# Kernel optimization log

Hardware: AMD Instinct MI355X
Metric: run time of the kernel (lower is better)

## Reference

```python
import jax, jax.numpy as jnp
import numpy as np
import math

N_TOTAL = 262144
C = 128
B = 512
LMAX = 512  # max segment length (static for jit)


def setup_inputs() -> dict:
    key = jax.random.key(0)
    ks = jax.random.split(key, 8)
    Q_feature = jax.random.normal(ks[0], (N_TOTAL, C), dtype=jnp.float32)
    K_feature = jax.random.normal(ks[1], (N_TOTAL, C), dtype=jnp.float32)
    # cumulative offsets: equal segments of length LMAX (general code handles ragged)
    offset = (jnp.arange(1, B + 1, dtype=jnp.int64) * (N_TOTAL // B))
    s = 1.0 / math.sqrt(C)
    Wq = jax.random.normal(ks[2], (C, C), dtype=jnp.float32) * s
    Wk = jax.random.normal(ks[3], (C, C), dtype=jnp.float32) * s
    Wv = jax.random.normal(ks[4], (C, C), dtype=jnp.float32) * s
    bq = jnp.zeros((C,), dtype=jnp.float32)
    bk = jnp.zeros((C,), dtype=jnp.float32)
    bv = jnp.zeros((C,), dtype=jnp.float32)
    return {"Q_feature": Q_feature, "K_feature": K_feature,
            "Wq": Wq, "bq": bq, "Wk": Wk, "bk": bk, "Wv": Wv, "bv": bv,
            "offset": offset}


def reference(Q_feature, K_feature, Wq, bq, Wk, bk, Wv, bv, offset):
    N, Cdim = Q_feature.shape
    Q = Q_feature @ Wq.T + bq
    K = K_feature @ Wk.T + bk
    V = K_feature @ Wv.T + bv

    starts = jnp.concatenate([jnp.zeros((1,), offset.dtype), offset[:-1]])
    lengths = offset - starts                         # (B,)
    pos = jnp.arange(LMAX)                            # (LMAX,)
    idx = jnp.clip(starts[:, None] + pos[None, :], 0, N - 1)  # (B, LMAX)
    mask = pos[None, :] < lengths[:, None]            # (B, LMAX) valid tokens

    Qp = Q[idx]                                       # (B, LMAX, C)
    Kp = K[idx]
    Vp = V[idx]

    scale = 1.0 / math.sqrt(Cdim)
    scores = jnp.einsum('blc,bmc->blm', Qp, Kp) * scale     # (B, LMAX, LMAX)
    scores = jnp.where(mask[:, None, :], scores, jnp.float32(-1e30))
    attn = jax.nn.softmax(scores, axis=-1)
    outp = jnp.einsum('blm,bmc->blc', attn, Vp)             # (B, LMAX, C)
    outp = outp * mask[:, :, None]                          # zero padded rows

    # scatter padded segments back to flat (N, C); idx is an exact partition on valid rows
    out = jnp.zeros((N, Cdim), dtype=outp.dtype).at[idx].add(outp)
    return out
```

## Files before the change

### kernel.cpp

```cpp
#include <hip/hip_runtime.h>
#include <hip/hip_bf16.h>

#define CDIM 128
#define LMAXC 512
#define QBLK 128
#define KVBLK 64

#define QSCALE (0.08838834764831845f * 1.4426950408889634f)

typedef __attribute__((ext_vector_type(8))) short bf16x8;
typedef __attribute__((ext_vector_type(4))) short bf16x4;
typedef __attribute__((ext_vector_type(4))) float f32x4;

__device__ inline short f2bf(float f) {
    union { float f; unsigned u; } v; v.f = f;
    unsigned r = v.u + 0x7FFFu + ((v.u >> 16) & 1u);
    return (short)(r >> 16);
}

__device__ inline bf16x8 cvt8v(float4 a, float4 b) {
    bf16x8 o;
    o[0] = f2bf(a.x); o[1] = f2bf(a.y); o[2] = f2bf(a.z); o[3] = f2bf(a.w);
    o[4] = f2bf(b.x); o[5] = f2bf(b.y); o[6] = f2bf(b.z); o[7] = f2bf(b.w);
    return o;
}

__device__ inline unsigned pk2(float lo, float hi) {
    unsigned r;
    asm("v_cvt_pk_bf16_f32 %0, %1, %2" : "=v"(r) : "v"(lo), "v"(hi));
    return r;
}

__device__ inline void gload16(const void* g, void* l) {
    __builtin_amdgcn_global_load_lds(
        (const __attribute__((address_space(1))) unsigned*)g,
        (__attribute__((address_space(3))) unsigned*)l, 16, 0, 0);
}

__device__ inline void blk_barrier() {
    __builtin_amdgcn_sched_barrier(0);
    __builtin_amdgcn_s_barrier();
    __builtin_amdgcn_sched_barrier(0);
}

__device__ inline int pch(int q) { return ((q + (q >> 3)) & 7) << 4; }

__global__ void wcvt_kernel(const float* __restrict__ Wq,
                            const float* __restrict__ Wk,
                            const float* __restrict__ Wv,
                            short* __restrict__ Wbf)
{
    int t = blockIdx.x * 256 + threadIdx.x;
    int m = t / 2048;
    int e = (t % 2048) * 8;
    const float* W = (m == 0) ? Wq : (m == 1) ? Wk : Wv;
    float sc = (m == 0) ? QSCALE : 1.0f;
    float4 a = *reinterpret_cast<const float4*>(W + e);
    float4 b = *reinterpret_cast<const float4*>(W + e + 4);
    a.x *= sc; a.y *= sc; a.z *= sc; a.w *= sc;
    b.x *= sc; b.y *= sc; b.z *= sc; b.w *= sc;
    *reinterpret_cast<bf16x8*>(Wbf + m * 16384 + e) = cvt8v(a, b);
}

__global__ __launch_bounds__(256) void proj_kernel(
    const float* __restrict__ Qf, const float* __restrict__ Kf,
    const short* __restrict__ Wbf,
    const float* __restrict__ bq, const float* __restrict__ bk,
    const float* __restrict__ bv,
    short* __restrict__ Qp, short* __restrict__ Kp, short* __restrict__ Vt,
    int N)
{
    __shared__ __align__(16) char wlds[32768];

    const int tid   = threadIdx.x;
    const int lane  = tid & 63;
    const int wv    = tid >> 6;
    const int lrow  = lane & 15;
    const int lhalf = lane >> 4;
    const int row0  = blockIdx.x * 128;
    const int which = blockIdx.y;
    const float* X  = (which == 0) ? Qf : Kf;
    const short* Wg = Wbf + which * 16384;

#pragma unroll
    for (int j = 0; j < 8; ++j) {
        int beta = j * 4096 + tid * 16;
        int r  = beta >> 8;
        int gs = ((beta >> 4) & 15) ^ (r & 7);
        gload16(Wg + r * 128 + gs * 8, wlds + beta);
    }

    bf16x8 xfr[2][4];
#pragma unroll
    for (int xt = 0; xt < 2; ++xt) {
        const float* xr = X + (size_t)(row0 + wv * 32 + xt * 16 + lrow) * CDIM;
#pragma unroll
        for (int ks = 0; ks < 4; ++ks) {
            const float4* s = reinterpret_cast<const float4*>(xr + ks * 32 + lhalf * 8);
            xfr[xt][ks] = cvt8v(s[0], s[1]);
        }
    }
    __syncthreads();

    if (which < 2) {
        const float* bias = (which == 0) ? bq : bk;
        const float  bsc  = (which == 0) ? QSCALE : 1.0f;
        short* outp       = (which == 0) ? Qp : Kp;

#pragma unroll
        for (int cf = 0; cf < 8; ++cf) {
            const int key = cf * 16 + lrow;
            bf16x8 wfr[4];
#pragma unroll
            for (int ks = 0; ks < 4; ++ks) {
                int wb = (key * 256 + (ks * 32 + lhalf * 8) * 2) ^ ((key & 7) << 4);
                wfr[ks] = *reinterpret_cast<const bf16x8*>(wlds + wb);
            }
            float4 bv4 = *reinterpret_cast<const float4*>(bias + cf * 16 + lhalf * 4);
#pragma unroll
            for (int xt = 0; xt < 2; ++xt) {
                f32x4 acc = {0.f, 0.f, 0.f, 0.f};
#pragma unroll
                for (int ks = 0; ks < 4; ++ks)
                    acc = __builtin_amdgcn_mfma_f32_16x16x32_bf16(wfr[ks], xfr[xt][ks], acc, 0, 0, 0);
                bf16x4 pk;
                pk[0] = f2bf(acc[0] + bv4.x * bsc);
                pk[1] = f2bf(acc[1] + bv4.y * bsc);
                pk[2] = f2bf(acc[2] + bv4.z * bsc);
                pk[3] = f2bf(acc[3] + bv4.w * bsc);
                *reinterpret_cast<bf16x4*>(
                    outp + (size_t)(row0 + wv * 32 + xt * 16 + lrow) * CDIM
                         + cf * 16 + lhalf * 4) = pk;
            }
        }
    } else {
#pragma unroll
        for (int cf = 0; cf < 8; ++cf) {
            const int d = cf * 16 + lrow;
            bf16x8 wfr[4];
#pragma unroll
            for (int ks = 0; ks < 4; ++ks) {
                int wb = (d * 256 + (ks * 32 + lhalf * 8) * 2) ^ ((d & 7) << 4);
                wfr[ks] = *reinterpret_cast<const bf16x8*>(wlds + wb);
            }
            f32x4 acc0 = {0.f, 0.f, 0.f, 0.f};
            f32x4 acc1 = {0.f, 0.f, 0.f, 0.f};
#pragma unroll
            for (int ks = 0; ks < 4; ++ks) {
                acc0 = __builtin_amdgcn_mfma_f32_16x16x32_bf16(xfr[0][ks], wfr[ks], acc0, 0, 0, 0);
                acc1 = __builtin_amdgcn_mfma_f32_16x16x32_bf16(xfr[1][ks], wfr[ks], acc1, 0, 0, 0);
            }
            float bcol = bv[d];
            bf16x4 p0, p1;
#pragma unroll
            for (int r = 0; r < 4; ++r) {
                p0[r] = f2bf(acc0[r] + bcol);
                p1[r] = f2bf(acc1[r] + bcol);
            }
            short* vrow = Vt + (size_t)d * N + row0 + wv * 32 + lhalf * 4;
            *reinterpret_cast<bf16x4*>(vrow)      = p0;
            *reinterpret_cast<bf16x4*>(vrow + 16) = p1;
        }
    }
}

__global__ __launch_bounds__(256) void attn_kernel(
    const short* __restrict__ Qp, const short* __restrict__ Kp,
    const short* __restrict__ VtG, const int* __restrict__ offset,
    float* __restrict__ out, int Ntot)
{
    __shared__ __align__(16) char smem[81920];
    char* lds_p = smem + 65536;

    const int nq = LMAXC / QBLK;
    int flat = blockIdx.x, total = gridDim.x;
    int seg, qb;
    if ((total & (8 * nq - 1)) == 0) {
        int per = total >> 3;
        int xcd = flat & 7;
        int wi  = flat >> 3;
        int sl  = wi / nq;
        qb  = wi - sl * nq;
        seg = xcd * (per / nq) + sl;
    } else { seg = flat / nq; qb = flat - seg * nq; }

    const int start = (seg == 0) ? 0 : offset[seg - 1];
    int len = offset[seg] - start;
    if (len > LMAXC) len = LMAXC;
    const int q0 = qb * QBLK;
    if (q0 >= len) return;

    const int tid   = threadIdx.x;
    const int lane  = tid & 63;
    const int wv    = tid >> 6;
    const int lrow  = lane & 15;
    const int lhalf = lane >> 4;
    const int ntiles = (len + KVBLK - 1) / KVBLK;
    const int lm1 = len - 1;

    auto stage = [&](int kv0, int bb) {
        char* kb = smem + bb * 32768;
        char* vb = kb + 16384;
#pragma unroll
        for (int j = 0; j < 4; ++j) {
            int beta = j * 4096 + wv * 1024 + (lane << 4);
            int r  = beta >> 8;
            int gs = ((beta >> 4) & 15) ^ (r & 7);
            int rg = kv0 + r; if (rg > lm1) rg = lm1;
            gload16(Kp + (((size_t)(start + rg)) << 7) + (gs << 3),
                    kb + j * 4096 + wv * 1024);
            int d   = beta >> 7;
            int gs2 = ((beta >> 4) & 7) ^ (d & 7);
            long gk = (long)start + kv0 + (gs2 << 3);
            if (gk + 8 > Ntot) gk = Ntot - 8;
            gload16(VtG + (size_t)d * Ntot + gk,
                    vb + j * 4096 + wv * 1024);
        }
    };

    stage(0, 0);

    bf16x8 aq[2][4];
#pragma unroll
    for (int qt = 0; qt < 2; ++qt) {
        int qr = q0 + wv * 32 + qt * 16 + lrow;
        if (qr > lm1) qr = lm1;
        const short* qrow = Qp + (size_t)(start + qr) * CDIM;
#pragma unroll
        for (int ks = 0; ks < 4; ++ks)
            aq[qt][ks] = *reinterpret_cast<const bf16x8*>(qrow + ks * 32 + lhalf * 8);
    }

    f32x4 acc_o[2][8];
    float lsum[2] = {0.f, 0.f};
#pragma unroll
    for (int qt = 0; qt < 2; ++qt)
#pragma unroll
        for (int df = 0; df < 8; ++df) acc_o[qt][df] = (f32x4){0.f, 0.f, 0.f, 0.f};

    const int wbase = wv * 4096;

    for (int t = 0; t < ntiles; ++t) {
        const int kv0 = t * KVBLK;
        const int bb  = t & 1;
        if (t + 1 < ntiles) {
            stage(kv0 + KVBLK, bb ^ 1);
            asm volatile("s_waitcnt vmcnt(8)" ::: "memory");
        } else {
            asm volatile("s_waitcnt vmcnt(0)" ::: "memory");
        }
        blk_barrier();

        char* lds_k  = smem + bb * 32768;
        char* lds_vt = lds_k + 16384;
        const bool tail = (kv0 + KVBLK > len);

        f32x4 s0[4], s1[4];
        __builtin_amdgcn_s_setprio(1);
#pragma unroll
        for (int kf = 0; kf < 4; ++kf) {
            s0[kf] = (f32x4){0.f, 0.f, 0.f, 0.f};
            s1[kf] = (f32x4){0.f, 0.f, 0.f, 0.f};
            int key = kf * 16 + lrow;
#pragma unroll
            for (int ks = 0; ks < 4; ++ks) {
                int kbo = (key * 256 + (ks * 32 + lhalf * 8) * 2) ^ ((key & 7) << 4);
                bf16x8 kfr = *reinterpret_cast<const bf16x8*>(lds_k + kbo);
                s0[kf] = __builtin_amdgcn_mfma_f32_16x16x32_bf16(kfr, aq[0][ks], s0[kf], 0, 0, 0);
                s1[kf] = __builtin_amdgcn_mfma_f32_16x16x32_bf16(kfr, aq[1][ks], s1[kf], 0, 0, 0);
            }
        }
        __builtin_amdgcn_s_setprio(0);

        const int keyb0 = kv0 + lhalf * 4;
#pragma unroll
        for (int qt = 0; qt < 2; ++qt) {
            const int qlocal = qt * 16 + lrow;
            const int rowoff = wbase + qlocal * 128;
            const int swz = pch(qlocal);
#pragma unroll
            for (int kf = 0; kf < 4; ++kf) {
                f32x4 sv = qt ? s1[kf] : s0[kf];
                float p[4];
#pragma unroll
                for (int r = 0; r < 4; ++r) {
                    float pv = exp2f(sv[r]);
                    if (tail && (keyb0 + kf * 16 + r >= len)) pv = 0.f;
                    p[r] = pv;
                    lsum[qt] += pv;
                }
                unsigned long long w =
                    (unsigned long long)pk2(p[0], p[1]) |
                    ((unsigned long long)pk2(p[2], p[3]) << 32);
                *reinterpret_cast<unsigned long long*>(
                    lds_p + rowoff + ((kf * 32 + lhalf * 8) ^ swz)) = w;
            }
        }

        __builtin_amdgcn_s_setprio(1);
#pragma unroll
        for (int ks2 = 0; ks2 < 2; ++ks2) {
            bf16x8 ap0 = *reinterpret_cast<const bf16x8*>(
                lds_p + wbase + lrow * 128 + ((ks2 * 64 + lhalf * 16) ^ pch(lrow)));
            bf16x8 ap1 = *reinterpret_cast<const bf16x8*>(
                lds_p + wbase + (16 + lrow) * 128 + ((ks2 * 64 + lhalf * 16) ^ pch(16 + lrow)));
            int k0 = ks2 * 32 + lhalf * 8;
#pragma unroll
            for (int df = 0; df < 8; ++df) {
                int d = df * 16 + lrow;
                int vb2 = (d * 128 + k0 * 2) ^ ((d & 7) << 4);
                bf16x8 bvf = *reinterpret_cast<const bf16x8*>(lds_vt + vb2);
                acc_o[0][df] = __builtin_amdgcn_mfma_f32_16x16x32_bf16(ap0, bvf, acc_o[0][df], 0, 0, 0);
                acc_o[1][df] = __builtin_amdgcn_mfma_f32_16x16x32_bf16(ap1, bvf, acc_o[1][df], 0, 0, 0);
            }
        }
        __builtin_amdgcn_s_setprio(0);

        blk_barrier();
    }

#pragma unroll
    for (int qt = 0; qt < 2; ++qt) {
        float l = lsum[qt];
        l += __shfl_xor(l, 16);
        l += __shfl_xor(l, 32);
        float rinv[4];
#pragma unroll
        for (int r = 0; r < 4; ++r)
            rinv[r] = 1.0f / __shfl(l, lhalf * 4 + r);
#pragma unroll
        for (int df = 0; df < 8; ++df)
#pragma unroll
            for (int r = 0; r < 4; ++r) {
                int qg = q0 + wv * 32 + qt * 16 + lhalf * 4 + r;
                if (qg < len)
                    out[(size_t)(start + qg) * CDIM + df * 16 + lrow]
                        = acc_o[qt][df][r] * rinv[r];
            }
    }
}

extern "C" void kernel_launch(void* const* d_in, const int* in_sizes, int n_in,
                              void* d_out, int out_size, void* d_ws, size_t ws_size,
                              hipStream_t stream) {
    const float* Qf = (const float*)d_in[0];
    const float* Kf = (const float*)d_in[1];
    const float* Wq = (const float*)d_in[2];
    const float* bq = (const float*)d_in[3];
    const float* Wk = (const float*)d_in[4];
    const float* bk = (const float*)d_in[5];
    const float* Wv = (const float*)d_in[6];
    const float* bv_ = (const float*)d_in[7];
    const int* offset = (const int*)d_in[8];

    const int N = in_sizes[0] / CDIM;
    const int B = in_sizes[8];

    short* Qp = (short*)d_ws;
    short* Kp = Qp + (size_t)N * CDIM;
    short* Vt = Kp + (size_t)N * CDIM;
    float* out = (float*)d_out;

    size_t base_need = (size_t)3 * N * CDIM * 2;
    short* Wbf = (ws_size >= base_need + 3 * 16384 * 2)
               ? (Vt + (size_t)N * CDIM) : (short*)d_out;

    wcvt_kernel<<<24, 256, 0, stream>>>(Wq, Wk, Wv, Wbf);

    dim3 pgrid(N / 128, 3);
    proj_kernel<<<pgrid, 256, 0, stream>>>(Qf, Kf, Wbf, bq, bk, bv_,
                                           Qp, Kp, Vt, N);

    attn_kernel<<<dim3(B * (LMAXC / QBLK)), 256, 0, stream>>>(
        Qp, Kp, Vt, offset, out, N);
}
```

Before: 254.0 us.

## Process four row tiles per projection block with software-prefetched inputs

Each projection block now handles 512 rows instead of 128. The weight tile staged in LDS is reused across four 128-row tiles, and the grid shrinks by four. The next tile's fp32 input is loaded into registers while MFMAs run on the current tile, so global load latency overlaps compute. The cost is higher register pressure from the raw float4 buffer, which may lower occupancy, and fewer blocks are available to fill the GPU.

```diff
diff --git a/kernel.cpp b/kernel.cpp
--- a/kernel.cpp
+++ b/kernel.cpp
@@ -62,6 +62,98 @@
     *reinterpret_cast<bf16x8*>(Wbf + m * 16384 + e) = cvt8v(a, b);
 }
 
+__device__ inline void loadraw(const float* __restrict__ X, int rowbase,
+                               int lrow, int lhalf, float4* raw)
+{
+#pragma unroll
+    for (int xt = 0; xt < 2; ++xt) {
+        const float* xr = X + (size_t)(rowbase + xt * 16 + lrow) * CDIM + lhalf * 8;
+#pragma unroll
+        for (int ks = 0; ks < 4; ++ks) {
+            raw[xt * 8 + ks * 2 + 0] = *reinterpret_cast<const float4*>(xr + ks * 32);
+            raw[xt * 8 + ks * 2 + 1] = *reinterpret_cast<const float4*>(xr + ks * 32 + 4);
+        }
+    }
+}
+
+__device__ inline void cvtraw(const float4* raw, bf16x8 xfr[2][4])
+{
+#pragma unroll
+    for (int xt = 0; xt < 2; ++xt)
+#pragma unroll
+        for (int ks = 0; ks < 4; ++ks)
+            xfr[xt][ks] = cvt8v(raw[xt * 8 + ks * 2], raw[xt * 8 + ks * 2 + 1]);
+}
+
+__device__ inline void tile_qk(const char* __restrict__ wlds,
+                               const bf16x8 xfr[2][4],
+                               const float* __restrict__ bias, float bsc,
+                               short* __restrict__ outp, int row0t,
+                               int lrow, int lhalf, int wv)
+{
+#pragma unroll
+    for (int cf = 0; cf < 8; ++cf) {
+        const int key = cf * 16 + lrow;
+        bf16x8 wfr[4];
+#pragma unroll
+        for (int ks = 0; ks < 4; ++ks) {
+            int wb = (key * 256 + (ks * 32 + lhalf * 8) * 2) ^ ((key & 7) << 4);
+            wfr[ks] = *reinterpret_cast<const bf16x8*>(wlds + wb);
+        }
+        float4 bv4 = *reinterpret_cast<const float4*>(bias + cf * 16 + lhalf * 4);
+#pragma unroll
+        for (int xt = 0; xt < 2; ++xt) {
+            f32x4 acc = {0.f, 0.f, 0.f, 0.f};
+#pragma unroll
+            for (int ks = 0; ks < 4; ++ks)
+                acc = __builtin_amdgcn_mfma_f32_16x16x32_bf16(wfr[ks], xfr[xt][ks], acc, 0, 0, 0);
+            bf16x4 pk;
+            pk[0] = f2bf(acc[0] + bv4.x * bsc);
+            pk[1] = f2bf(acc[1] + bv4.y * bsc);
+            pk[2] = f2bf(acc[2] + bv4.z * bsc);
+            pk[3] = f2bf(acc[3] + bv4.w * bsc);
+            *reinterpret_cast<bf16x4*>(
+                outp + (size_t)(row0t + wv * 32 + xt * 16 + lrow) * CDIM
+                     + cf * 16 + lhalf * 4) = pk;
+        }
+    }
+}
+
+__device__ inline void tile_v(const char* __restrict__ wlds,
+                              const bf16x8 xfr[2][4],
+                              const float* __restrict__ bv,
+                              short* __restrict__ Vt, int row0t, int N,
+                              int lrow, int lhalf, int wv)
+{
+#pragma unroll
+    for (int cf = 0; cf < 8; ++cf) {
+        const int d = cf * 16 + lrow;
+        bf16x8 wfr[4];
+#pragma unroll
+        for (int ks = 0; ks < 4; ++ks) {
+            int wb = (d * 256 + (ks * 32 + lhalf * 8) * 2) ^ ((d & 7) << 4);
+            wfr[ks] = *reinterpret_cast<const bf16x8*>(wlds + wb);
+        }
+        f32x4 acc0 = {0.f, 0.f, 0.f, 0.f};
+        f32x4 acc1 = {0.f, 0.f, 0.f, 0.f};
+#pragma unroll
+        for (int ks = 0; ks < 4; ++ks) {
+            acc0 = __builtin_amdgcn_mfma_f32_16x16x32_bf16(xfr[0][ks], wfr[ks], acc0, 0, 0, 0);
+            acc1 = __builtin_amdgcn_mfma_f32_16x16x32_bf16(xfr[1][ks], wfr[ks], acc1, 0, 0, 0);
+        }
+        float bcol = bv[d];
+        bf16x4 p0, p1;
+#pragma unroll
+        for (int r = 0; r < 4; ++r) {
+            p0[r] = f2bf(acc0[r] + bcol);
+            p1[r] = f2bf(acc1[r] + bcol);
+        }
+        short* vrow = Vt + (size_t)d * N + row0t + wv * 32 + lhalf * 4;
+        *reinterpret_cast<bf16x4*>(vrow)      = p0;
+        *reinterpret_cast<bf16x4*>(vrow + 16) = p1;
+    }
+}
+
 __global__ __launch_bounds__(256) void proj_kernel(
     const float* __restrict__ Qf, const float* __restrict__ Kf,
     const short* __restrict__ Wbf,
@@ -77,7 +169,7 @@
     const int wv    = tid >> 6;
     const int lrow  = lane & 15;
     const int lhalf = lane >> 4;
-    const int row0  = blockIdx.x * 128;
+    const int row0  = blockIdx.x * 512;
     const int which = blockIdx.y;
     const float* X  = (which == 0) ? Qf : Kf;
     const short* Wg = Wbf + which * 16384;
@@ -90,76 +182,32 @@
         gload16(Wg + r * 128 + gs * 8, wlds + beta);
     }
 
+    float4 raw[16];
     bf16x8 xfr[2][4];
-#pragma unroll
-    for (int xt = 0; xt < 2; ++xt) {
-        const float* xr = X + (size_t)(row0 + wv * 32 + xt * 16 + lrow) * CDIM;
-#pragma unroll
-        for (int ks = 0; ks < 4; ++ks) {
-            const float4* s = reinterpret_cast<const float4*>(xr + ks * 32 + lhalf * 8);
-            xfr[xt][ks] = cvt8v(s[0], s[1]);
-        }
-    }
+    loadraw(X, row0 + wv * 32, lrow, lhalf, raw);
+    cvtraw(raw, xfr);
     __syncthreads();
 
-    if (which < 2) {
-        const float* bias = (which == 0) ? bq : bk;
-        const float  bsc  = (which == 0) ? QSCALE : 1.0f;
-        short* outp       = (which == 0) ? Qp : Kp;
-
-#pragma unroll
-        for (int cf = 0; cf < 8; ++cf) {
-            const int key = cf * 16 + lrow;
-            bf16x8 wfr[4];
-#pragma unroll
-            for (int ks = 0; ks < 4; ++ks) {
-                int wb = (key * 256 + (ks * 32 + lhalf * 8) * 2) ^ ((key & 7) << 4);
-                wfr[ks] = *reinterpret_cast<const bf16x8*>(wlds + wb);
-            }
-            float4 bv4 = *reinterpret_cast<const float4*>(bias + cf * 16 + lhalf * 4);
-#pragma unroll
-            for (int xt = 0; xt < 2; ++xt) {
-                f32x4 acc = {0.f, 0.f, 0.f, 0.f};
-#pragma unroll
-                for (int ks = 0; ks < 4; ++ks)
-                    acc = __builtin_amdgcn_mfma_f32_16x16x32_bf16(wfr[ks], xfr[xt][ks], acc, 0, 0, 0);
-                bf16x4 pk;
-                pk[0] = f2bf(acc[0] + bv4.x * bsc);
-                pk[1] = f2bf(acc[1] + bv4.y * bsc);
-                pk[2] = f2bf(acc[2] + bv4.z * bsc);
-                pk[3] = f2bf(acc[3] + bv4.w * bsc);
-                *reinterpret_cast<bf16x4*>(
-                    outp + (size_t)(row0 + wv * 32 + xt * 16 + lrow) * CDIM
-                         + cf * 16 + lhalf * 4) = pk;
-            }
+    if (which == 0) {
+#pragma unroll
+        for (int t = 0; t < 4; ++t) {
+            if (t < 3) loadraw(X, row0 + (t + 1) * 128 + wv * 32, lrow, lhalf, raw);
+            tile_qk(wlds, xfr, bq, QSCALE, Qp, row0 + t * 128, lrow, lhalf, wv);
+            if (t < 3) cvtraw(raw, xfr);
+        }
+    } else if (which == 1) {
+#pragma unroll
+        for (int t = 0; t < 4; ++t) {
+            if (t < 3) loadraw(X, row0 + (t + 1) * 128 + wv * 32, lrow, lhalf, raw);
+            tile_qk(wlds, xfr, bk, 1.0f, Kp, row0 + t * 128, lrow, lhalf, wv);
+            if (t < 3) cvtraw(raw, xfr);
         }
     } else {
 #pragma unroll
-        for (int cf = 0; cf < 8; ++cf) {
-            const int d = cf * 16 + lrow;
-            bf16x8 wfr[4];
-#pragma unroll
-            for (int ks = 0; ks < 4; ++ks) {
-                int wb = (d * 256 + (ks * 32 + lhalf * 8) * 2) ^ ((d & 7) << 4);
-                wfr[ks] = *reinterpret_cast<const bf16x8*>(wlds + wb);
-            }
-            f32x4 acc0 = {0.f, 0.f, 0.f, 0.f};
-            f32x4 acc1 = {0.f, 0.f, 0.f, 0.f};
-#pragma unroll
-            for (int ks = 0; ks < 4; ++ks) {
-                acc0 = __builtin_amdgcn_mfma_f32_16x16x32_bf16(xfr[0][ks], wfr[ks], acc0, 0, 0, 0);
-                acc1 = __builtin_amdgcn_mfma_f32_16x16x32_bf16(xfr[1][ks], wfr[ks], acc1, 0, 0, 0);
-            }
-            float bcol = bv[d];
-            bf16x4 p0, p1;
-#pragma unroll
-            for (int r = 0; r < 4; ++r) {
-                p0[r] = f2bf(acc0[r] + bcol);
-                p1[r] = f2bf(acc1[r] + bcol);
-            }
-            short* vrow = Vt + (size_t)d * N + row0 + wv * 32 + lhalf * 4;
-            *reinterpret_cast<bf16x4*>(vrow)      = p0;
-            *reinterpret_cast<bf16x4*>(vrow + 16) = p1;
+        for (int t = 0; t < 4; ++t) {
+            if (t < 3) loadraw(X, row0 + (t + 1) * 128 + wv * 32, lrow, lhalf, raw);
+            tile_v(wlds, xfr, bv, Vt, row0 + t * 128, N, lrow, lhalf, wv);
+            if (t < 3) cvtraw(raw, xfr);
         }
     }
 }
@@ -367,7 +415,7 @@
 
     wcvt_kernel<<<24, 256, 0, stream>>>(Wq, Wk, Wv, Wbf);
 
-    dim3 pgrid(N / 128, 3);
+    dim3 pgrid(N / 512, 3);
     proj_kernel<<<pgrid, 256, 0, stream>>>(Qf, Kf, Wbf, bq, bk, bv_,
                                            Qp, Kp, Vt, N);
 
```

Result: slower. 282.4 us (+11.2%).

## Fuse K and V projections to reuse K_feature loads, use 512-thread blocks

Applied to the files above, without the earlier changes.

The projection kernel previously ran three grid slices (Q, K, V), each loading and converting its input rows from fp32. K and V both read K_feature, so that data was fetched twice. The K-slice blocks now compute K, reload the Wv tile into LDS after a barrier, and compute V from the same register-resident fragments, which removes the redundant read. Blocks also grow to 512 threads covering 256 rows. The cost is an extra LDS reload and two barriers in the K/V blocks, plus an uneven workload between Q blocks and K/V blocks.

```diff
diff --git a/kernel.cpp b/kernel.cpp
--- a/kernel.cpp
+++ b/kernel.cpp
@@ -62,7 +62,76 @@
     *reinterpret_cast<bf16x8*>(Wbf + m * 16384 + e) = cvt8v(a, b);
 }
 
-__global__ __launch_bounds__(256) void proj_kernel(
+__device__ inline void tile_qk(const char* __restrict__ wlds,
+                               const bf16x8 xfr[2][4],
+                               const float* __restrict__ bias, float bsc,
+                               short* __restrict__ outp, int rowb,
+                               int lrow, int lhalf)
+{
+#pragma unroll
+    for (int cf = 0; cf < 8; ++cf) {
+        const int key = cf * 16 + lrow;
+        bf16x8 wfr[4];
+#pragma unroll
+        for (int ks = 0; ks < 4; ++ks) {
+            int wb = (key * 256 + (ks * 32 + lhalf * 8) * 2) ^ ((key & 7) << 4);
+            wfr[ks] = *reinterpret_cast<const bf16x8*>(wlds + wb);
+        }
+        float4 bv4 = *reinterpret_cast<const float4*>(bias + cf * 16 + lhalf * 4);
+#pragma unroll
+        for (int xt = 0; xt < 2; ++xt) {
+            f32x4 acc = {0.f, 0.f, 0.f, 0.f};
+#pragma unroll
+            for (int ks = 0; ks < 4; ++ks)
+                acc = __builtin_amdgcn_mfma_f32_16x16x32_bf16(wfr[ks], xfr[xt][ks], acc, 0, 0, 0);
+            bf16x4 pk;
+            pk[0] = f2bf(acc[0] + bv4.x * bsc);
+            pk[1] = f2bf(acc[1] + bv4.y * bsc);
+            pk[2] = f2bf(acc[2] + bv4.z * bsc);
+            pk[3] = f2bf(acc[3] + bv4.w * bsc);
+            *reinterpret_cast<bf16x4*>(
+                outp + (size_t)(rowb + xt * 16 + lrow) * CDIM
+                     + cf * 16 + lhalf * 4) = pk;
+        }
+    }
+}
+
+__device__ inline void tile_v(const char* __restrict__ wlds,
+                              const bf16x8 xfr[2][4],
+                              const float* __restrict__ bv,
+                              short* __restrict__ Vt, int rowb, int N,
+                              int lrow, int lhalf)
+{
+#pragma unroll
+    for (int cf = 0; cf < 8; ++cf) {
+        const int d = cf * 16 + lrow;
+        bf16x8 wfr[4];
+#pragma unroll
+        for (int ks = 0; ks < 4; ++ks) {
+            int wb = (d * 256 + (ks * 32 + lhalf * 8) * 2) ^ ((d & 7) << 4);
+            wfr[ks] = *reinterpret_cast<const bf16x8*>(wlds + wb);
+        }
+        f32x4 acc0 = {0.f, 0.f, 0.f, 0.f};
+        f32x4 acc1 = {0.f, 0.f, 0.f, 0.f};
+#pragma unroll
+        for (int ks = 0; ks < 4; ++ks) {
+            acc0 = __builtin_amdgcn_mfma_f32_16x16x32_bf16(xfr[0][ks], wfr[ks], acc0, 0, 0, 0);
+            acc1 = __builtin_amdgcn_mfma_f32_16x16x32_bf16(xfr[1][ks], wfr[ks], acc1, 0, 0, 0);
+        }
+        float bcol = bv[d];
+        bf16x4 p0, p1;
+#pragma unroll
+        for (int r = 0; r < 4; ++r) {
+            p0[r] = f2bf(acc0[r] + bcol);
+            p1[r] = f2bf(acc1[r] + bcol);
+        }
+        short* vrow = Vt + (size_t)d * N + rowb + lhalf * 4;
+        *reinterpret_cast<bf16x4*>(vrow)      = p0;
+        *reinterpret_cast<bf16x4*>(vrow + 16) = p1;
+    }
+}
+
+__global__ __launch_bounds__(512) void proj_kernel(
     const float* __restrict__ Qf, const float* __restrict__ Kf,
     const short* __restrict__ Wbf,
     const float* __restrict__ bq, const float* __restrict__ bk,
@@ -77,14 +146,15 @@
     const int wv    = tid >> 6;
     const int lrow  = lane & 15;
     const int lhalf = lane >> 4;
-    const int row0  = blockIdx.x * 128;
-    const int which = blockIdx.y;
-    const float* X  = (which == 0) ? Qf : Kf;
-    const short* Wg = Wbf + which * 16384;
-
-#pragma unroll
-    for (int j = 0; j < 8; ++j) {
-        int beta = j * 4096 + tid * 16;
+    const int row0  = blockIdx.x * 256;
+    const bool isQ  = (blockIdx.y == 0);
+    const float* X  = isQ ? Qf : Kf;
+    const int rowb  = row0 + wv * 32;
+
+    const short* Wg = isQ ? Wbf : Wbf + 16384;
+#pragma unroll
+    for (int j = 0; j < 4; ++j) {
+        int beta = j * 8192 + tid * 16;
         int r  = beta >> 8;
         int gs = ((beta >> 4) & 15) ^ (r & 7);
         gload16(Wg + r * 128 + gs * 8, wlds + beta);
@@ -93,74 +163,29 @@
     bf16x8 xfr[2][4];
 #pragma unroll
     for (int xt = 0; xt < 2; ++xt) {
-        const float* xr = X + (size_t)(row0 + wv * 32 + xt * 16 + lrow) * CDIM;
+        const float* xr = X + (size_t)(rowb + xt * 16 + lrow) * CDIM + lhalf * 8;
 #pragma unroll
         for (int ks = 0; ks < 4; ++ks) {
-            const float4* s = reinterpret_cast<const float4*>(xr + ks * 32 + lhalf * 8);
+            const float4* s = reinterpret_cast<const float4*>(xr + ks * 32);
             xfr[xt][ks] = cvt8v(s[0], s[1]);
         }
     }
     __syncthreads();
 
-    if (which < 2) {
-        const float* bias = (which == 0) ? bq : bk;
-        const float  bsc  = (which == 0) ? QSCALE : 1.0f;
-        short* outp       = (which == 0) ? Qp : Kp;
-
-#pragma unroll
-        for (int cf = 0; cf < 8; ++cf) {
-            const int key = cf * 16 + lrow;
-            bf16x8 wfr[4];
-#pragma unroll
-            for (int ks = 0; ks < 4; ++ks) {
-                int wb = (key * 256 + (ks * 32 + lhalf * 8) * 2) ^ ((key & 7) << 4);
-                wfr[ks] = *reinterpret_cast<const bf16x8*>(wlds + wb);
-            }
-            float4 bv4 = *reinterpret_cast<const float4*>(bias + cf * 16 + lhalf * 4);
-#pragma unroll
-            for (int xt = 0; xt < 2; ++xt) {
-                f32x4 acc = {0.f, 0.f, 0.f, 0.f};
-#pragma unroll
-                for (int ks = 0; ks < 4; ++ks)
-                    acc = __builtin_amdgcn_mfma_f32_16x16x32_bf16(wfr[ks], xfr[xt][ks], acc, 0, 0, 0);
-                bf16x4 pk;
-                pk[0] = f2bf(acc[0] + bv4.x * bsc);
-                pk[1] = f2bf(acc[1] + bv4.y * bsc);
-                pk[2] = f2bf(acc[2] + bv4.z * bsc);
-                pk[3] = f2bf(acc[3] + bv4.w * bsc);
-                *reinterpret_cast<bf16x4*>(
-                    outp + (size_t)(row0 + wv * 32 + xt * 16 + lrow) * CDIM
-                         + cf * 16 + lhalf * 4) = pk;
-            }
-        }
+    if (isQ) {
+        tile_qk(wlds, xfr, bq, QSCALE, Qp, rowb, lrow, lhalf);
     } else {
-#pragma unroll
-        for (int cf = 0; cf < 8; ++cf) {
-            const int d = cf * 16 + lrow;
-            bf16x8 wfr[4];
-#pragma unroll
-            for (int ks = 0; ks < 4; ++ks) {
-                int wb = (d * 256 + (ks * 32 + lhalf * 8) * 2) ^ ((d & 7) << 4);
-                wfr[ks] = *reinterpret_cast<const bf16x8*>(wlds + wb);
-            }
-            f32x4 acc0 = {0.f, 0.f, 0.f, 0.f};
-            f32x4 acc1 = {0.f, 0.f, 0.f, 0.f};
-#pragma unroll
-            for (int ks = 0; ks < 4; ++ks) {
-                acc0 = __builtin_amdgcn_mfma_f32_16x16x32_bf16(xfr[0][ks], wfr[ks], acc0, 0, 0, 0);
-                acc1 = __builtin_amdgcn_mfma_f32_16x16x32_bf16(xfr[1][ks], wfr[ks], acc1, 0, 0, 0);
-            }
-            float bcol = bv[d];
-            bf16x4 p0, p1;
-#pragma unroll
-            for (int r = 0; r < 4; ++r) {
-                p0[r] = f2bf(acc0[r] + bcol);
-                p1[r] = f2bf(acc1[r] + bcol);
-            }
-            short* vrow = Vt + (size_t)d * N + row0 + wv * 32 + lhalf * 4;
-            *reinterpret_cast<bf16x4*>(vrow)      = p0;
-            *reinterpret_cast<bf16x4*>(vrow + 16) = p1;
-        }
+        tile_qk(wlds, xfr, bk, 1.0f, Kp, rowb, lrow, lhalf);
+        __syncthreads();
+#pragma unroll
+        for (int j = 0; j < 4; ++j) {
+            int beta = j * 8192 + tid * 16;
+            int r  = beta >> 8;
+            int gs = ((beta >> 4) & 15) ^ (r & 7);
+            gload16(Wbf + 32768 + r * 128 + gs * 8, wlds + beta);
+        }
+        __syncthreads();
+        tile_v(wlds, xfr, bv, Vt, rowb, N, lrow, lhalf);
     }
 }
 
@@ -367,8 +392,8 @@
 
     wcvt_kernel<<<24, 256, 0, stream>>>(Wq, Wk, Wv, Wbf);
 
-    dim3 pgrid(N / 128, 3);
-    proj_kernel<<<pgrid, 256, 0, stream>>>(Qf, Kf, Wbf, bq, bk, bv_,
+    dim3 pgrid(N / 256, 2);
+    proj_kernel<<<pgrid, 512, 0, stream>>>(Qf, Kf, Wbf, bq, bk, bv_,
                                            Qp, Kp, Vt, N);
 
     attn_kernel<<<dim3(B * (LMAXC / QBLK)), 256, 0, stream>>>(
```

New measurement: 249.5 us. About the same (-1.8%).
